# Kernel optimization log

Hardware: AMD Instinct MI355X
Metric: run time of the kernel (lower is better)

Reference implementation:

```python
import jax, jax.numpy as jnp
import numpy as np

T, N, E, G = 2, 100000, 1600000, 512
IN, DIM, LIN, OUT = 6, 36, 54, 18
BN_EPS = 1e-5


def setup_inputs() -> dict:
    key = jax.random.key(0)
    ks = iter(jax.random.split(key, 64))
    nrm = lambda shape, s=0.1: jax.random.normal(next(ks), shape, jnp.float32) * s
    inp = {
        'x': jax.random.normal(next(ks), (T, N, IN), jnp.float32),
        'edge_index': jax.random.randint(next(ks), (T, 2, E), 0, N),
        'batch': jnp.sort(jax.random.randint(next(ks), (T, N), 0, G), axis=-1),
        # GINConv MLPs per transform (conv1: IN->DIM->DIM, conv2/3: DIM->DIM->DIM)
        'w1a': nrm((T, DIM, IN)), 'b1a': jnp.zeros((T, DIM)),
        'w1b': nrm((T, DIM, DIM)), 'b1b': jnp.zeros((T, DIM)),
        'w2a': nrm((T, DIM, DIM)), 'b2a': jnp.zeros((T, DIM)),
        'w2b': nrm((T, DIM, DIM)), 'b2b': jnp.zeros((T, DIM)),
        'w3a': nrm((T, DIM, DIM)), 'b3a': jnp.zeros((T, DIM)),
        'w3b': nrm((T, DIM, DIM)), 'b3b': jnp.zeros((T, DIM)),
        # BatchNorm affine params, 3 BNs per transform
        'bn_g': jnp.ones((T, 3, DIM)), 'bn_b': jnp.zeros((T, 3, DIM)),
        # head: Linear(2*DIM -> LIN), Linear(LIN -> OUT), Linear(OUT -> 1)
        'hw1': nrm((LIN, T * DIM)), 'hb1': jnp.zeros((LIN,)),
        'hw2': nrm((OUT, LIN)), 'hb2': jnp.zeros((OUT,)),
        'hw3': nrm((1, OUT)), 'hb3': jnp.zeros((1,)),
    }
    return inp


def _gin_conv(h, src, dst, wa, ba, wb, bb):
    # GINConv (eps=0): nn((1+eps)*x + sum_{j in N(i)} x_j)
    agg = jax.ops.segment_sum(h[src], dst, num_segments=N)  # [N, d]
    h = h + agg
    h = jax.nn.relu(h @ wa.T + ba)
    return h @ wb.T + bb


def _bn(h, g, b):
    # training-mode BatchNorm1d over node axis (biased variance, eps=1e-5)
    mu = h.mean(0)
    var = h.var(0)
    return g * (h - mu) * jax.lax.rsqrt(var + BN_EPS) + b


def reference(x, edge_index, batch, w1a, b1a, w1b, b1b, w2a, b2a, w2b, b2b,
              w3a, b3a, w3b, b3b, bn_g, bn_b, hw1, hb1, hw2, hb2, hw3, hb3):
    embeds = []
    for t in range(T):  # fixed small number of structurally distinct branches
        src, dst = edge_index[t, 0], edge_index[t, 1]
        h = x[t]
        h = _bn(jax.nn.relu(_gin_conv(h, src, dst, w1a[t], b1a[t], w1b[t], b1b[t])), bn_g[t, 0], bn_b[t, 0])
        h = _bn(jax.nn.relu(_gin_conv(h, src, dst, w2a[t], b2a[t], w2b[t], b2b[t])), bn_g[t, 1], bn_b[t, 1])
        h = _bn(jax.nn.relu(_gin_conv(h, src, dst, w3a[t], b3a[t], w3b[t], b3b[t])), bn_g[t, 2], bn_b[t, 2])
        # global_mean_pool over graph ids
        sums = jax.ops.segment_sum(h, batch[t], num_segments=G)  # [G, DIM]
        cnts = jax.ops.segment_sum(jnp.ones((N,), h.dtype), batch[t], num_segments=G)
        embeds.append(sums / jnp.maximum(cnts, 1.0)[:, None])
    emb = jnp.concatenate(embeds, axis=1)  # [G, T*DIM]
    h = jax.nn.relu(emb @ hw1.T + hb1)
    h = jax.nn.relu(h @ hw2.T + hb2)
    # dropout(p=0.1) treated as eval/identity for a deterministic reference
    return jax.nn.sigmoid(h @ hw3.T + hb3)  # [G, 1]
```

## Files before the change

### kernel.cpp

```cpp
#include <hip/hip_runtime.h>

#define T_   2
#define IN_  6
#define DIM_ 36
#define LIN_ 54
#define OUT_ 18
#define BN_EPS 1e-5f

#define WSH_   7
#define WMSK_  127
#define CAP_   2560
#define TILE_  12288
#define NBMAX_ 1024

__device__ __forceinline__ unsigned short f2bf(float f) {
    unsigned u = __float_as_uint(f);
    unsigned r = (u + 0x7FFFu + ((u >> 16) & 1u)) >> 16;
    return (unsigned short)r;
}
__device__ __forceinline__ float bf2f(unsigned short h) {
    return __uint_as_float(((unsigned)h) << 16);
}
__device__ __forceinline__ unsigned packbf(float a, float b) {
    return (unsigned)f2bf(a) | ((unsigned)f2bf(b) << 16);
}

__global__ __launch_bounds__(256) void binsort_k(
    const int* __restrict__ ei, int t0, int gbin,
    int* __restrict__ bcnt, int* __restrict__ bbuf, int ne, int nb)
{
    __shared__ int cntl[NBMAX_], cursl[NBMAX_], gbasel[NBMAX_];
    __shared__ int aux[256];
    __shared__ int sortedl[TILE_];

    const int tid  = threadIdx.x;
    const int lt   = blockIdx.x / gbin;
    const int tile = blockIdx.x % gbin;
    const int base = tile * TILE_;
    const int cnt_e = min(TILE_, ne - base);
    const int* srcp = ei + (size_t)(t0 + lt) * 2 * ne;
    const int* dstp = srcp + ne;
    int* bcnt_t = bcnt + (size_t)lt * nb;

    for (int i = tid; i < NBMAX_; i += 256) cntl[i] = 0;
    __syncthreads();

    for (int i = tid; i < cnt_e; i += 256)
        atomicAdd(&cntl[dstp[base + i] >> WSH_], 1);
    __syncthreads();

    int t4 = tid * 4;
    int c0 = cntl[t4+0], c1 = cntl[t4+1], c2 = cntl[t4+2], c3 = cntl[t4+3];
    int lsum = c0 + c1 + c2 + c3;
    aux[tid] = lsum;
    __syncthreads();
    for (int off = 1; off < 256; off <<= 1) {
        int v = (tid >= off) ? aux[tid - off] : 0;
        __syncthreads();
        aux[tid] += v;
        __syncthreads();
    }
    int eb = aux[tid] - lsum;
    cursl[t4+0] = eb;
    cursl[t4+1] = eb + c0;
    cursl[t4+2] = eb + c0 + c1;
    cursl[t4+3] = eb + c0 + c1 + c2;
    __syncthreads();

    for (int b = tid; b < nb; b += 256) {
        int c = cntl[b];
        gbasel[b] = c ? atomicAdd(&bcnt_t[b], c) : 0;
    }
    __syncthreads();

    for (int i = tid; i < cnt_e; i += 256) {
        int s = srcp[base + i], d = dstp[base + i];
        int p = atomicAdd(&cursl[d >> WSH_], 1);
        sortedl[p] = s | ((d & WMSK_) << 17);
    }
    __syncthreads();

    int grp16 = tid >> 4, ln16 = tid & 15;
    for (int b = grp16; b < nb; b += 16) {
        int c = cntl[b];
        if (!c) continue;
        int lb = cursl[b] - c;
        int gb = gbasel[b];
        size_t ga = ((size_t)lt * nb + b) * CAP_ + gb;
        for (int i = ln16; i < c; i += 16)
            if (gb + i < CAP_) bbuf[ga + i] = sortedl[lb + i];
    }
}

__global__ __launch_bounds__(256) void csrify_k(
    const int* __restrict__ bcnt, int* __restrict__ bbuf,
    int* __restrict__ rp, int* __restrict__ deg, int n, int nb)
{
    __shared__ int ent[CAP_], srt[CAP_];
    __shared__ int cnt[128], cur[128], sc[128];
    const int b = blockIdx.x, tid = threadIdx.x;
    const int blocal = b % nb, lt = b / nb;
    int c = min(bcnt[b], CAP_);
    int* seg = bbuf + (size_t)b * CAP_;

    for (int i = tid; i < c; i += 256) ent[i] = seg[i];
    if (tid < 128) cnt[tid] = 0;
    __syncthreads();
    for (int i = tid; i < c; i += 256)
        atomicAdd(&cnt[(ent[i] >> 17) & WMSK_], 1);
    __syncthreads();
    if (tid < 128) sc[tid] = cnt[tid];
    __syncthreads();
    for (int off = 1; off < 128; off <<= 1) {
        int v = (tid >= off && tid < 128) ? sc[tid - off] : 0;
        __syncthreads();
        if (tid < 128) sc[tid] += v;
        __syncthreads();
    }
    int node0 = blocal << WSH_;
    if (tid < 128) {
        int excl = sc[tid] - cnt[tid];
        cur[tid] = excl;
        if (node0 + tid < n) {
            rp[(size_t)lt * n + node0 + tid]  = b * CAP_ + excl;
            deg[(size_t)lt * n + node0 + tid] = cnt[tid];
        }
    }
    __syncthreads();
    for (int i = tid; i < c; i += 256) {
        int v = ent[i];
        int p = atomicAdd(&cur[(v >> 17) & WMSK_], 1);
        srt[p] = v & 0x1FFFF;
    }
    __syncthreads();
    for (int i = tid; i < c; i += 256) seg[i] = srt[i];
}

template<int D>
__global__ __launch_bounds__(576) void gather_k(
        const float* __restrict__ hbase, size_t hstride,
        const int* __restrict__ rp, const int* __restrict__ deg,
        const int* __restrict__ csr, float* __restrict__ agg,
        size_t astride, int n)
{
    const int NPB = 576 / D;
    const int slot = blockIdx.y;
    const float* h = hbase + (size_t)slot * hstride;
    int g = blockIdx.x * NPB + threadIdx.x / D;
    int lane = threadIdx.x % D;
    if (g >= n) return;
    int lo = rp[(size_t)slot * n + g], hi = lo + deg[(size_t)slot * n + g];
    float a0 = h[(size_t)g * D + lane], a1 = 0.f, a2 = 0.f, a3 = 0.f;
    int e = lo;
    for (; e + 3 < hi; e += 4) {
        int s0 = csr[e], s1 = csr[e + 1], s2 = csr[e + 2], s3 = csr[e + 3];
        a0 += h[(size_t)s0 * D + lane];
        a1 += h[(size_t)s1 * D + lane];
        a2 += h[(size_t)s2 * D + lane];
        a3 += h[(size_t)s3 * D + lane];
    }
    for (; e < hi; ++e) a0 += h[(size_t)csr[e] * D + lane];
    agg[(size_t)slot * astride + (size_t)g * D + lane] = (a0 + a1) + (a2 + a3);
}

__global__ __launch_bounds__(576) void gather36h_k(
        const unsigned short* __restrict__ zh, size_t zhstride,
        const int* __restrict__ rp, const int* __restrict__ deg,
        const int* __restrict__ csr, float* __restrict__ agg,
        size_t astride, int n)
{
    const int slot = blockIdx.y;
    const unsigned short* zhs = zh + (size_t)slot * zhstride;
    int g = blockIdx.x * 64 + threadIdx.x / 9;
    int lane = threadIdx.x % 9;
    if (g >= n) return;
    size_t off = (size_t)slot * n + g;
    int lo = rp[off], hi = lo + deg[off];

    uint2 v = *reinterpret_cast<const uint2*>(zhs + (size_t)g * DIM_ + 4 * lane);
    float a0 = bf2f((unsigned short)(v.x & 0xffff));
    float a1 = bf2f((unsigned short)(v.x >> 16));
    float a2 = bf2f((unsigned short)(v.y & 0xffff));
    float a3 = bf2f((unsigned short)(v.y >> 16));
    float b0 = 0.f, b1 = 0.f, b2 = 0.f, b3 = 0.f;

    int e = lo;
    for (; e + 1 < hi; e += 2) {
        int s0 = csr[e], s1 = csr[e + 1];
        uint2 u0 = *reinterpret_cast<const uint2*>(zhs + (size_t)s0 * DIM_ + 4 * lane);
        uint2 u1 = *reinterpret_cast<const uint2*>(zhs + (size_t)s1 * DIM_ + 4 * lane);
        a0 += bf2f((unsigned short)(u0.x & 0xffff));
        a1 += bf2f((unsigned short)(u0.x >> 16));
        a2 += bf2f((unsigned short)(u0.y & 0xffff));
        a3 += bf2f((unsigned short)(u0.y >> 16));
        b0 += bf2f((unsigned short)(u1.x & 0xffff));
        b1 += bf2f((unsigned short)(u1.x >> 16));
        b2 += bf2f((unsigned short)(u1.y & 0xffff));
        b3 += bf2f((unsigned short)(u1.y >> 16));
    }
    if (e < hi) {
        uint2 u0 = *reinterpret_cast<const uint2*>(zhs + (size_t)csr[e] * DIM_ + 4 * lane);
        a0 += bf2f((unsigned short)(u0.x & 0xffff));
        a1 += bf2f((unsigned short)(u0.x >> 16));
        a2 += bf2f((unsigned short)(u0.y & 0xffff));
        a3 += bf2f((unsigned short)(u0.y >> 16));
    }
    float4 r; r.x = a0 + b0; r.y = a1 + b1; r.z = a2 + b2; r.w = a3 + b3;
    *reinterpret_cast<float4*>(agg + (size_t)slot * astride + (size_t)g * DIM_ + 4 * lane) = r;
}

__global__ __launch_bounds__(256) void node6_k(
    const float* __restrict__ agg, size_t astride,
    const float* __restrict__ wAb, const float* __restrict__ bAb,
    const float* __restrict__ wBb, const float* __restrict__ bBb,
    int t0,
    unsigned short* __restrict__ zho, size_t zstride,
    float* __restrict__ bstats, int gn, int n)
{
    __shared__ float sstat[4][2 * DIM_];
    const int slot = blockIdx.y;
    const int t = t0 + slot;
    const float* wa = wAb + (size_t)t * DIM_ * IN_;
    const float* ba = bAb + (size_t)t * DIM_;
    const float* wb = wBb + (size_t)t * DIM_ * DIM_;
    const float* bb = bBb + (size_t)t * DIM_;

    int node = blockIdx.x * 256 + threadIdx.x;
    bool active = node < n;

    float hin[IN_];
    if (active) {
        const float2* ar2 = reinterpret_cast<const float2*>(
                agg + (size_t)slot * astride + (size_t)node * IN_);
        float2 v0 = ar2[0], v1 = ar2[1], v2 = ar2[2];
        hin[0] = v0.x; hin[1] = v0.y; hin[2] = v1.x;
        hin[3] = v1.y; hin[4] = v2.x; hin[5] = v2.y;
    } else {
        #pragma unroll
        for (int k = 0; k < IN_; ++k) hin[k] = 0.f;
    }

    float y[DIM_];
    #pragma unroll
    for (int j = 0; j < DIM_; ++j) {
        float acc = ba[j];
        #pragma unroll
        for (int k = 0; k < IN_; ++k) acc = fmaf(wa[j * IN_ + k], hin[k], acc);
        y[j] = fmaxf(acc, 0.f);
    }
    float out[DIM_];
    #pragma unroll
    for (int j = 0; j < DIM_; ++j) {
        float acc = bb[j];
        #pragma unroll
        for (int k = 0; k < DIM_; ++k) acc = fmaf(wb[j * DIM_ + k], y[k], acc);
        out[j] = active ? fmaxf(acc, 0.f) : 0.f;
    }

    if (active) {
        unsigned* zr = reinterpret_cast<unsigned*>(
                zho + (size_t)slot * zstride + (size_t)node * DIM_);
        #pragma unroll
        for (int j = 0; j < DIM_ / 2; ++j) zr[j] = packbf(out[2*j], out[2*j+1]);
    }

    int wid = threadIdx.x >> 6, lane = threadIdx.x & 63;
    #pragma unroll
    for (int j = 0; j < DIM_; ++j) {
        float s = out[j], sq = out[j] * out[j];
        for (int off = 32; off; off >>= 1) {
            s  += __shfl_down(s,  off);
            sq += __shfl_down(sq, off);
        }
        if (lane == 0) { sstat[wid][j] = s; sstat[wid][DIM_ + j] = sq; }
    }
    __syncthreads();
    if (threadIdx.x < 2 * DIM_) {
        float s = sstat[0][threadIdx.x] + sstat[1][threadIdx.x]
                + sstat[2][threadIdx.x] + sstat[3][threadIdx.x];
        bstats[((size_t)slot * gn + blockIdx.x) * (2 * DIM_) + threadIdx.x] = s;
    }
}

__global__ __launch_bounds__(256) void node36_k(
    const float* __restrict__ agg, size_t astride,
    const int* __restrict__ deg,
    const float* __restrict__ coef,
    const float* __restrict__ wAb, const float* __restrict__ bAb,
    const float* __restrict__ wBb, const float* __restrict__ bBb,
    int t0,
    unsigned short* __restrict__ zho, size_t zstride,
    float* __restrict__ bstats, int gn, int n)
{
    __shared__ float sstat[4][2 * DIM_];
    const int slot = blockIdx.y;
    const int t = t0 + slot;
    const float* wa = wAb + (size_t)t * DIM_ * DIM_;
    const float* ba = bAb + (size_t)t * DIM_;
    const float* wb = wBb + (size_t)t * DIM_ * DIM_;
    const float* bb = bBb + (size_t)t * DIM_;
    const float* ca  = coef + (size_t)slot * 2 * DIM_;
    const float* cb2 = ca + DIM_;

    int node = blockIdx.x * 256 + threadIdx.x;
    bool active = node < n;

    float hin[DIM_];
    if (active) {
        const float4* ar4 = reinterpret_cast<const float4*>(
                agg + (size_t)slot * astride + (size_t)node * DIM_);
        #pragma unroll
        for (int q = 0; q < 9; ++q) {
            float4 av = ar4[q];
            hin[4*q+0] = av.x; hin[4*q+1] = av.y;
            hin[4*q+2] = av.z; hin[4*q+3] = av.w;
        }
        float ds = 1.0f + (float)deg[(size_t)slot * n + node];
        #pragma unroll
        for (int k = 0; k < DIM_; ++k)
            hin[k] = ca[k] * hin[k] + ds * cb2[k];
    } else {
        #pragma unroll
        for (int k = 0; k < DIM_; ++k) hin[k] = 0.f;
    }

    float y[DIM_];
    #pragma unroll
    for (int j = 0; j < DIM_; ++j) {
        float acc = ba[j];
        #pragma unroll
        for (int k = 0; k < DIM_; ++k) acc = fmaf(wa[j * DIM_ + k], hin[k], acc);
        y[j] = fmaxf(acc, 0.f);
    }
    float out[DIM_];
    #pragma unroll
    for (int j = 0; j < DIM_; ++j) {
        float acc = bb[j];
        #pragma unroll
        for (int k = 0; k < DIM_; ++k) acc = fmaf(wb[j * DIM_ + k], y[k], acc);
        out[j] = active ? fmaxf(acc, 0.f) : 0.f;
    }

    if (active) {
        unsigned* zr = reinterpret_cast<unsigned*>(
                zho + (size_t)slot * zstride + (size_t)node * DIM_);
        #pragma unroll
        for (int j = 0; j < DIM_ / 2; ++j) zr[j] = packbf(out[2*j], out[2*j+1]);
    }

    int wid = threadIdx.x >> 6, lane = threadIdx.x & 63;
    #pragma unroll
    for (int j = 0; j < DIM_; ++j) {
        float s = out[j], sq = out[j] * out[j];
        for (int off = 32; off; off >>= 1) {
            s  += __shfl_down(s,  off);
            sq += __shfl_down(sq, off);
        }
        if (lane == 0) { sstat[wid][j] = s; sstat[wid][DIM_ + j] = sq; }
    }
    __syncthreads();
    if (threadIdx.x < 2 * DIM_) {
        float s = sstat[0][threadIdx.x] + sstat[1][threadIdx.x]
                + sstat[2][threadIdx.x] + sstat[3][threadIdx.x];
        bstats[((size_t)slot * gn + blockIdx.x) * (2 * DIM_) + threadIdx.x] = s;
    }
}

__global__ __launch_bounds__(288) void bnfin_k(
    const float* __restrict__ bstats, int nrows, int rstride,
    const float* __restrict__ bng, const float* __restrict__ bnb,
    int t0, int c, float* __restrict__ coef, float inv_n)
{
    __shared__ float part[4][2 * DIM_];
    const int slot = blockIdx.x;
    const int t = t0 + slot;
    int tid = threadIdx.x;
    int col = tid % (2 * DIM_), quarter = tid / (2 * DIM_);
    const float* bs = bstats + (size_t)slot * rstride * (2 * DIM_);
    float s = 0.f;
    for (int i = quarter; i < nrows; i += 4) s += bs[(size_t)i * (2 * DIM_) + col];
    part[quarter][col] = s;
    __syncthreads();
    if (tid < 2 * DIM_)
        part[0][tid] = part[0][tid] + part[1][tid] + part[2][tid] + part[3][tid];
    __syncthreads();
    if (tid < DIM_) {
        float mean = part[0][tid] * inv_n;
        float var  = part[0][DIM_ + tid] * inv_n - mean * mean;
        float aa   = bng[((size_t)t * 3 + c) * DIM_ + tid] / sqrtf(var + BN_EPS);
        coef[(size_t)slot * 2 * DIM_ + tid]        = aa;
        coef[(size_t)slot * 2 * DIM_ + DIM_ + tid] = bnb[((size_t)t * 3 + c) * DIM_ + tid] - aa * mean;
    }
}

__global__ __launch_bounds__(288) void pool_k(
    const unsigned short* __restrict__ zh, size_t zstride,
    const float* __restrict__ coef,
    const int* __restrict__ batch, int t0,
    float* __restrict__ emb, int n)
{
    __shared__ int slo, shi;
    __shared__ float sp0[16][19], sp1[16][19];
    const int slot = blockIdx.y;
    const int t = t0 + slot;
    const int* bt = batch + (size_t)t * n;
    const unsigned short* zt = zh + (size_t)slot * zstride;
    const float* ca  = coef + (size_t)slot * 2 * DIM_;
    const float* cb2 = ca + DIM_;

    int g = blockIdx.x;
    int tid = threadIdx.x;
    if (tid == 0) {
        int lo = 0, hi = n;
        while (lo < hi) { int m = (lo + hi) >> 1; if (bt[m] < g) lo = m + 1; else hi = m; }
        slo = lo;
        int lo2 = lo, hi2 = n;
        while (lo2 < hi2) { int m = (lo2 + hi2) >> 1; if (bt[m] < g + 1) lo2 = m + 1; else hi2 = m; }
        shi = lo2;
    }
    __syncthreads();
    int lo = slo, hi = shi;
    int fp = tid % 18, j = tid / 18;
    float acc0 = 0.f, acc1 = 0.f;
    for (int i = lo + j; i < hi; i += 16) {
        unsigned v = *reinterpret_cast<const unsigned*>(zt + (size_t)i * DIM_ + 2 * fp);
        acc0 += bf2f((unsigned short)(v & 0xffff));
        acc1 += bf2f((unsigned short)(v >> 16));
    }
    sp0[j][fp] = acc0;
    sp1[j][fp] = acc1;
    __syncthreads();
    if (tid < DIM_) {
        int f = tid, fpair = f >> 1, hi_ = f & 1;
        float s = 0.f;
        #pragma unroll
        for (int jj = 0; jj < 16; ++jj)
            s += hi_ ? sp1[jj][fpair] : sp0[jj][fpair];
        int cnt = hi - lo;
        float val = 0.f;
        if (cnt > 0) val = ca[f] * (s / (float)cnt) + cb2[f];
        emb[(size_t)g * (T_ * DIM_) + t * DIM_ + f] = val;
    }
}

__global__ __launch_bounds__(64) void head_k(
    const float* __restrict__ emb,
    const float* __restrict__ hw1, const float* __restrict__ hb1,
    const float* __restrict__ hw2, const float* __restrict__ hb2,
    const float* __restrict__ hw3, const float* __restrict__ hb3,
    float* __restrict__ out, int ng)
{
    const int EMB = T_ * DIM_;
    int g = blockIdx.x;
    if (g >= ng) return;
    __shared__ float se[EMB], st1[LIN_], st2[OUT_];
    int tid = threadIdx.x;
    for (int i = tid; i < EMB; i += 64) se[i] = emb[(size_t)g * EMB + i];
    __syncthreads();
    if (tid < LIN_) {
        float acc = hb1[tid];
        #pragma unroll
        for (int k = 0; k < EMB; ++k) acc = fmaf(hw1[tid * EMB + k], se[k], acc);
        st1[tid] = fmaxf(acc, 0.f);
    }
    __syncthreads();
    if (tid < OUT_) {
        float acc = hb2[tid];
        #pragma unroll
        for (int k = 0; k < LIN_; ++k) acc = fmaf(hw2[tid * LIN_ + k], st1[k], acc);
        st2[tid] = fmaxf(acc, 0.f);
    }
    __syncthreads();
    if (tid == 0) {
        float acc = hb3[0];
        #pragma unroll
        for (int k = 0; k < OUT_; ++k) acc = fmaf(hw3[k], st2[k], acc);
        out[g] = 1.f / (1.f + expf(-acc));
    }
}

extern "C" void kernel_launch(void* const* d_in, const int* in_sizes, int n_in,
                              void* d_out, int out_size, void* d_ws, size_t ws_size,
                              hipStream_t stream)
{
    const float* x     = (const float*)d_in[0];
    const int*   ei    = (const int*)d_in[1];
    const int*   batch = (const int*)d_in[2];
    const float* wA[3] = {(const float*)d_in[3], (const float*)d_in[7], (const float*)d_in[11]};
    const float* bA[3] = {(const float*)d_in[4], (const float*)d_in[8], (const float*)d_in[12]};
    const float* wB[3] = {(const float*)d_in[5], (const float*)d_in[9], (const float*)d_in[13]};
    const float* bB[3] = {(const float*)d_in[6], (const float*)d_in[10], (const float*)d_in[14]};
    const float* bng = (const float*)d_in[15];
    const float* bnb = (const float*)d_in[16];
    const float* hw1 = (const float*)d_in[17];
    const float* hb1 = (const float*)d_in[18];
    const float* hw2 = (const float*)d_in[19];
    const float* hb2 = (const float*)d_in[20];
    const float* hw3 = (const float*)d_in[21];
    const float* hb3 = (const float*)d_in[22];

    const int N = in_sizes[2] / T_;
    const int E = in_sizes[1] / (2 * T_);
    const int G = out_size;
    const int NB = (N + WMSK_) / 128;
    const int gn = (N + 255) / 256;
    const float inv_n = 1.0f / (float)N;
    const int gbin = (E + TILE_ - 1) / TILE_;

    const size_t bufN = (size_t)N * DIM_;
    auto need = [&](int tc) -> size_t {
        size_t f = (size_t)tc * bufN
                 + (size_t)tc * gn * 2 * DIM_
                 + (size_t)tc * 2 * DIM_
                 + (size_t)G * T_ * DIM_;
        size_t hs = 2 * (size_t)tc * bufN;
        size_t ii = (size_t)tc * NB + 2 * (size_t)tc * N + (size_t)tc * NB * CAP_;
        return f * sizeof(float) + hs * sizeof(unsigned short) + ii * sizeof(int);
    };
    const int tcnt = (need(2) <= ws_size) ? 2 : 1;

    char* ws = (char*)d_ws;
    float* agg    = (float*)ws;
    float* bstats = agg + (size_t)tcnt * bufN;
    float* coef   = bstats + (size_t)tcnt * gn * 2 * DIM_;
    float* emb    = coef + (size_t)tcnt * 2 * DIM_;
    unsigned short* zhA = (unsigned short*)(emb + (size_t)G * T_ * DIM_);
    unsigned short* zhB = zhA + (size_t)tcnt * bufN;
    int*   bcnt   = (int*)(zhB + (size_t)tcnt * bufN);
    int*   rp     = bcnt + (size_t)tcnt * NB;
    int*   deg    = rp + (size_t)tcnt * N;
    int*   bbuf   = deg + (size_t)tcnt * N;

    float* outp = (float*)d_out;

    for (int t0 = 0; t0 < T_; t0 += tcnt) {
        const int tc = tcnt;

        hipMemsetAsync(bcnt, 0, (size_t)tc * NB * sizeof(int), stream);
        binsort_k<<<tc * gbin, 256, 0, stream>>>(ei, t0, gbin, bcnt, bbuf, E, NB);
        csrify_k<<<tc * NB, 256, 0, stream>>>(bcnt, bbuf, rp, deg, N, NB);

        gather_k<IN_><<<dim3((N + 95) / 96, tc), 576, 0, stream>>>(
                x + (size_t)t0 * N * IN_, (size_t)N * IN_,
                rp, deg, bbuf, agg, (size_t)N * IN_, N);
        node6_k<<<dim3(gn, tc), 256, 0, stream>>>(
                agg, (size_t)N * IN_, wA[0], bA[0], wB[0], bB[0], t0,
                zhA, bufN, bstats, gn, N);
        bnfin_k<<<tc, 288, 0, stream>>>(bstats, gn, gn, bng, bnb, t0, 0, coef, inv_n);

        gather36h_k<<<dim3((N + 63) / 64, tc), 576, 0, stream>>>(
                zhA, bufN, rp, deg, bbuf, agg, bufN, N);
        node36_k<<<dim3(gn, tc), 256, 0, stream>>>(
                agg, bufN, deg, coef, wA[1], bA[1], wB[1], bB[1], t0,
                zhB, bufN, bstats, gn, N);
        bnfin_k<<<tc, 288, 0, stream>>>(bstats, gn, gn, bng, bnb, t0, 1, coef, inv_n);

        gather36h_k<<<dim3((N + 63) / 64, tc), 576, 0, stream>>>(
                zhB, bufN, rp, deg, bbuf, agg, bufN, N);
        node36_k<<<dim3(gn, tc), 256, 0, stream>>>(
                agg, bufN, deg, coef, wA[2], bA[2], wB[2], bB[2], t0,
                zhA, bufN, bstats, gn, N);
        bnfin_k<<<tc, 288, 0, stream>>>(bstats, gn, gn, bng, bnb, t0, 2, coef, inv_n);

        pool_k<<<dim3(G, tc), 288, 0, stream>>>(zhA, bufN, coef, batch, t0, emb, N);
    }
    head_k<<<G, 64, 0, stream>>>(emb, hw1, hb1, hw2, hb2, hw3, hb3, outp, G);
}
```

Measured before the change: 483.1 us.

## Split per-node MLP across four threads per node with shuffle exchange

```diff
diff --git a/kernel.cpp b/kernel.cpp
--- a/kernel.cpp
+++ b/kernel.cpp
@@ -209,80 +209,8 @@
     *reinterpret_cast<float4*>(agg + (size_t)slot * astride + (size_t)g * DIM_ + 4 * lane) = r;
 }
 
-__global__ __launch_bounds__(256) void node6_k(
-    const float* __restrict__ agg, size_t astride,
-    const float* __restrict__ wAb, const float* __restrict__ bAb,
-    const float* __restrict__ wBb, const float* __restrict__ bBb,
-    int t0,
-    unsigned short* __restrict__ zho, size_t zstride,
-    float* __restrict__ bstats, int gn, int n)
-{
-    __shared__ float sstat[4][2 * DIM_];
-    const int slot = blockIdx.y;
-    const int t = t0 + slot;
-    const float* wa = wAb + (size_t)t * DIM_ * IN_;
-    const float* ba = bAb + (size_t)t * DIM_;
-    const float* wb = wBb + (size_t)t * DIM_ * DIM_;
-    const float* bb = bBb + (size_t)t * DIM_;
-
-    int node = blockIdx.x * 256 + threadIdx.x;
-    bool active = node < n;
-
-    float hin[IN_];
-    if (active) {
-        const float2* ar2 = reinterpret_cast<const float2*>(
-                agg + (size_t)slot * astride + (size_t)node * IN_);
-        float2 v0 = ar2[0], v1 = ar2[1], v2 = ar2[2];
-        hin[0] = v0.x; hin[1] = v0.y; hin[2] = v1.x;
-        hin[3] = v1.y; hin[4] = v2.x; hin[5] = v2.y;
-    } else {
-        #pragma unroll
-        for (int k = 0; k < IN_; ++k) hin[k] = 0.f;
-    }
-
-    float y[DIM_];
-    #pragma unroll
-    for (int j = 0; j < DIM_; ++j) {
-        float acc = ba[j];
-        #pragma unroll
-        for (int k = 0; k < IN_; ++k) acc = fmaf(wa[j * IN_ + k], hin[k], acc);
-        y[j] = fmaxf(acc, 0.f);
-    }
-    float out[DIM_];
-    #pragma unroll
-    for (int j = 0; j < DIM_; ++j) {
-        float acc = bb[j];
-        #pragma unroll
-        for (int k = 0; k < DIM_; ++k) acc = fmaf(wb[j * DIM_ + k], y[k], acc);
-        out[j] = active ? fmaxf(acc, 0.f) : 0.f;
-    }
-
-    if (active) {
-        unsigned* zr = reinterpret_cast<unsigned*>(
-                zho + (size_t)slot * zstride + (size_t)node * DIM_);
-        #pragma unroll
-        for (int j = 0; j < DIM_ / 2; ++j) zr[j] = packbf(out[2*j], out[2*j+1]);
-    }
-
-    int wid = threadIdx.x >> 6, lane = threadIdx.x & 63;
-    #pragma unroll
-    for (int j = 0; j < DIM_; ++j) {
-        float s = out[j], sq = out[j] * out[j];
-        for (int off = 32; off; off >>= 1) {
-            s  += __shfl_down(s,  off);
-            sq += __shfl_down(sq, off);
-        }
-        if (lane == 0) { sstat[wid][j] = s; sstat[wid][DIM_ + j] = sq; }
-    }
-    __syncthreads();
-    if (threadIdx.x < 2 * DIM_) {
-        float s = sstat[0][threadIdx.x] + sstat[1][threadIdx.x]
-                + sstat[2][threadIdx.x] + sstat[3][threadIdx.x];
-        bstats[((size_t)slot * gn + blockIdx.x) * (2 * DIM_) + threadIdx.x] = s;
-    }
-}
-
-__global__ __launch_bounds__(256) void node36_k(
+template<int DIN, bool AFF>
+__global__ __launch_bounds__(256) void node_q(
     const float* __restrict__ agg, size_t astride,
     const int* __restrict__ deg,
     const float* __restrict__ coef,
@@ -295,74 +223,105 @@
     __shared__ float sstat[4][2 * DIM_];
     const int slot = blockIdx.y;
     const int t = t0 + slot;
-    const float* wa = wAb + (size_t)t * DIM_ * DIM_;
+    const float* wa = wAb + (size_t)t * DIM_ * DIN;
     const float* ba = bAb + (size_t)t * DIM_;
     const float* wb = wBb + (size_t)t * DIM_ * DIM_;
     const float* bb = bBb + (size_t)t * DIM_;
-    const float* ca  = coef + (size_t)slot * 2 * DIM_;
-    const float* cb2 = ca + DIM_;
-
-    int node = blockIdx.x * 256 + threadIdx.x;
-    bool active = node < n;
-
-    float hin[DIM_];
-    if (active) {
-        const float4* ar4 = reinterpret_cast<const float4*>(
-                agg + (size_t)slot * astride + (size_t)node * DIM_);
-        #pragma unroll
-        for (int q = 0; q < 9; ++q) {
-            float4 av = ar4[q];
-            hin[4*q+0] = av.x; hin[4*q+1] = av.y;
-            hin[4*q+2] = av.z; hin[4*q+3] = av.w;
+
+    const int tid = threadIdx.x;
+    const int grp = tid >> 2, p = tid & 3;
+    int node = blockIdx.x * 64 + grp;
+    bool act = node < n;
+
+    float hin[DIN];
+    if (act) {
+        const float* ar = agg + (size_t)slot * astride + (size_t)node * DIN;
+        if constexpr (DIN == 36) {
+            const float4* ar4 = reinterpret_cast<const float4*>(ar);
+            #pragma unroll
+            for (int q = 0; q < 9; ++q) {
+                float4 av = ar4[q];
+                hin[4*q+0] = av.x; hin[4*q+1] = av.y;
+                hin[4*q+2] = av.z; hin[4*q+3] = av.w;
+            }
+        } else {
+            const float2* ar2 = reinterpret_cast<const float2*>(ar);
+            #pragma unroll
+            for (int q = 0; q < DIN / 2; ++q) {
+                float2 av = ar2[q];
+                hin[2*q+0] = av.x; hin[2*q+1] = av.y;
+            }
         }
-        float ds = 1.0f + (float)deg[(size_t)slot * n + node];
-        #pragma unroll
-        for (int k = 0; k < DIM_; ++k)
-            hin[k] = ca[k] * hin[k] + ds * cb2[k];
+        if constexpr (AFF) {
+            const float* ca  = coef + (size_t)slot * 2 * DIM_;
+            const float* cb2 = ca + DIM_;
+            float ds = 1.0f + (float)deg[(size_t)slot * n + node];
+            #pragma unroll
+            for (int k = 0; k < DIN; ++k)
+                hin[k] = ca[k] * hin[k] + ds * cb2[k];
+        }
     } else {
         #pragma unroll
-        for (int k = 0; k < DIM_; ++k) hin[k] = 0.f;
-    }
-
-    float y[DIM_];
+        for (int k = 0; k < DIN; ++k) hin[k] = 0.f;
+    }
+
+    float yp[9];
     #pragma unroll
-    for (int j = 0; j < DIM_; ++j) {
+    for (int r = 0; r < 9; ++r) {
+        int j = 9 * p + r;
         float acc = ba[j];
         #pragma unroll
-        for (int k = 0; k < DIM_; ++k) acc = fmaf(wa[j * DIM_ + k], hin[k], acc);
-        y[j] = fmaxf(acc, 0.f);
-    }
-    float out[DIM_];
+        for (int k = 0; k < DIN; ++k) acc = fmaf(wa[j * DIN + k], hin[k], acc);
+        yp[r] = fmaxf(acc, 0.f);
+    }
+
+    float yf[DIM_];
+    int base = tid & ~3;
     #pragma unroll
-    for (int j = 0; j < DIM_; ++j) {
+    for (int m = 0; m < 4; ++m) {
+        #pragma unroll
+        for (int r = 0; r < 9; ++r)
+            yf[9 * m + r] = __shfl(yp[r], base + m);
+    }
+
+    float op[9];
+    #pragma unroll
+    for (int r = 0; r < 9; ++r) {
+        int j = 9 * p + r;
         float acc = bb[j];
         #pragma unroll
-        for (int k = 0; k < DIM_; ++k) acc = fmaf(wb[j * DIM_ + k], y[k], acc);
-        out[j] = active ? fmaxf(acc, 0.f) : 0.f;
-    }
-
-    if (active) {
-        unsigned* zr = reinterpret_cast<unsigned*>(
-                zho + (size_t)slot * zstride + (size_t)node * DIM_);
-        #pragma unroll
-        for (int j = 0; j < DIM_ / 2; ++j) zr[j] = packbf(out[2*j], out[2*j+1]);
-    }
-
-    int wid = threadIdx.x >> 6, lane = threadIdx.x & 63;
+        for (int k = 0; k < DIM_; ++k) acc = fmaf(wb[j * DIM_ + k], yf[k], acc);
+        op[r] = act ? fmaxf(acc, 0.f) : 0.f;
+    }
+
+    if (act) {
+        unsigned short* zr = zho + (size_t)slot * zstride + (size_t)node * DIM_ + 9 * p;
+        #pragma unroll
+        for (int r = 0; r < 9; ++r) zr[r] = f2bf(op[r]);
+    }
+
+    int wid = tid >> 6, lane = tid & 63;
+    float ss[9], sq[9];
     #pragma unroll
-    for (int j = 0; j < DIM_; ++j) {
-        float s = out[j], sq = out[j] * out[j];
-        for (int off = 32; off; off >>= 1) {
-            s  += __shfl_down(s,  off);
-            sq += __shfl_down(sq, off);
+    for (int r = 0; r < 9; ++r) { ss[r] = op[r]; sq[r] = op[r] * op[r]; }
+    #pragma unroll
+    for (int r = 0; r < 9; ++r) {
+        for (int off = 32; off >= 4; off >>= 1) {
+            ss[r] += __shfl_down(ss[r], off);
+            sq[r] += __shfl_down(sq[r], off);
         }
-        if (lane == 0) { sstat[wid][j] = s; sstat[wid][DIM_ + j] = sq; }
-    }
-    __syncthreads();
-    if (threadIdx.x < 2 * DIM_) {
-        float s = sstat[0][threadIdx.x] + sstat[1][threadIdx.x]
-                + sstat[2][threadIdx.x] + sstat[3][threadIdx.x];
-        bstats[((size_t)slot * gn + blockIdx.x) * (2 * DIM_) + threadIdx.x] = s;
+    }
+    if (lane < 4) {
+        #pragma unroll
+        for (int r = 0; r < 9; ++r) {
+            sstat[wid][9 * lane + r]        = ss[r];
+            sstat[wid][DIM_ + 9 * lane + r] = sq[r];
+        }
+    }
+    __syncthreads();
+    if (tid < 2 * DIM_) {
+        float s = sstat[0][tid] + sstat[1][tid] + sstat[2][tid] + sstat[3][tid];
+        bstats[((size_t)slot * gn + blockIdx.x) * (2 * DIM_) + tid] = s;
     }
 }
 
@@ -503,14 +462,14 @@
     const int E = in_sizes[1] / (2 * T_);
     const int G = out_size;
     const int NB = (N + WMSK_) / 128;
-    const int gn = (N + 255) / 256;
+    const int gnq = (N + 63) / 64;
     const float inv_n = 1.0f / (float)N;
     const int gbin = (E + TILE_ - 1) / TILE_;
 
     const size_t bufN = (size_t)N * DIM_;
     auto need = [&](int tc) -> size_t {
         size_t f = (size_t)tc * bufN
-                 + (size_t)tc * gn * 2 * DIM_
+                 + (size_t)tc * gnq * 2 * DIM_
                  + (size_t)tc * 2 * DIM_
                  + (size_t)G * T_ * DIM_;
         size_t hs = 2 * (size_t)tc * bufN;
@@ -522,7 +481,7 @@
     char* ws = (char*)d_ws;
     float* agg    = (float*)ws;
     float* bstats = agg + (size_t)tcnt * bufN;
-    float* coef   = bstats + (size_t)tcnt * gn * 2 * DIM_;
+    float* coef   = bstats + (size_t)tcnt * gnq * 2 * DIM_;
     float* emb    = coef + (size_t)tcnt * 2 * DIM_;
     unsigned short* zhA = (unsigned short*)(emb + (size_t)G * T_ * DIM_);
     unsigned short* zhB = zhA + (size_t)tcnt * bufN;
@@ -543,24 +502,27 @@
         gather_k<IN_><<<dim3((N + 95) / 96, tc), 576, 0, stream>>>(
                 x + (size_t)t0 * N * IN_, (size_t)N * IN_,
                 rp, deg, bbuf, agg, (size_t)N * IN_, N);
-        node6_k<<<dim3(gn, tc), 256, 0, stream>>>(
-                agg, (size_t)N * IN_, wA[0], bA[0], wB[0], bB[0], t0,
-                zhA, bufN, bstats, gn, N);
-        bnfin_k<<<tc, 288, 0, stream>>>(bstats, gn, gn, bng, bnb, t0, 0, coef, inv_n);
+        node_q<IN_, false><<<dim3(gnq, tc), 256, 0, stream>>>(
+                agg, (size_t)N * IN_, deg, nullptr,
+                wA[0], bA[0], wB[0], bB[0], t0,
+                zhA, bufN, bstats, gnq, N);
+        bnfin_k<<<tc, 288, 0, stream>>>(bstats, gnq, gnq, bng, bnb, t0, 0, coef, inv_n);
 
         gather36h_k<<<dim3((N + 63) / 64, tc), 576, 0, stream>>>(
                 zhA, bufN, rp, deg, bbuf, agg, bufN, N);
-        node36_k<<<dim3(gn, tc), 256, 0, stream>>>(
-                agg, bufN, deg, coef, wA[1], bA[1], wB[1], bB[1], t0,
-                zhB, bufN, bstats, gn, N);
-        bnfin_k<<<tc, 288, 0, stream>>>(bstats, gn, gn, bng, bnb, t0, 1, coef, inv_n);
+        node_q<DIM_, true><<<dim3(gnq, tc), 256, 0, stream>>>(
+                agg, bufN, deg, coef,
+                wA[1], bA[1], wB[1], bB[1], t0,
+                zhB, bufN, bstats, gnq, N);
+        bnfin_k<<<tc, 288, 0, stream>>>(bstats, gnq, gnq, bng, bnb, t0, 1, coef, inv_n);
 
         gather36h_k<<<dim3((N + 63) / 64, tc), 576, 0, stream>>>(
                 zhB, bufN, rp, deg, bbuf, agg, bufN, N);
-        node36_k<<<dim3(gn, tc), 256, 0, stream>>>(
-                agg, bufN, deg, coef, wA[2], bA[2], wB[2], bB[2], t0,
-                zhA, bufN, bstats, gn, N);
-        bnfin_k<<<tc, 288, 0, stream>>>(bstats, gn, gn, bng, bnb, t0, 2, coef, inv_n);
+        node_q<DIM_, true><<<dim3(gnq, tc), 256, 0, stream>>>(
+                agg, bufN, deg, coef,
+                wA[2], bA[2], wB[2], bB[2], t0,
+                zhA, bufN, bstats, gnq, N);
+        bnfin_k<<<tc, 288, 0, stream>>>(bstats, gnq, gnq, bng, bnb, t0, 2, coef, inv_n);
 
         pool_k<<<dim3(G, tc), 288, 0, stream>>>(zhA, bufN, coef, batch, t0, emb, N);
     }
```

Measured after the change: 864.2 us. +78.9%, slower.
